# Kernel tuning notes

Hardware: AMD Instinct MI355X
Metric: run time of the kernel (lower is better)

## Reference

```python
import jax, jax.numpy as jnp
import numpy as np
import math

D = 1024
H = 16
HD = D // H  # 64
SCALE = math.sqrt(HD)


def setup_inputs() -> dict:
    key = jax.random.key(0)
    ks = jax.random.split(key, 4)
    B, S = 2, 2048
    x = jax.random.normal(ks[0], (B, S, D), dtype=jnp.float32)
    attention_mask = jnp.zeros((B, S), dtype=jnp.float32)  # additive mask
    w_attn = jax.random.normal(ks[1], (D, 3 * D), dtype=jnp.float32) * (1.0 / math.sqrt(D))
    b_attn = jnp.zeros((3 * D,), dtype=jnp.float32)
    w_proj = jax.random.normal(ks[2], (D, D), dtype=jnp.float32) * (1.0 / math.sqrt(D))
    b_proj = jnp.zeros((D,), dtype=jnp.float32)
    return {"x": x, "attention_mask": attention_mask, "w_attn": w_attn,
            "b_attn": b_attn, "w_proj": w_proj, "b_proj": b_proj}


def reference(x, attention_mask, w_attn, b_attn, w_proj, b_proj):
    B, S, _ = x.shape
    qkv = x @ w_attn + b_attn                      # [B,S,3D]
    q, k, v = jnp.split(qkv, 3, axis=-1)           # each [B,S,D]
    # split heads -> [B,H,S,HD]
    sh = lambda t: t.reshape(B, S, H, HD).transpose(0, 2, 1, 3)
    q, k, v = sh(q), sh(k), sh(v)
    scores = jnp.einsum('bhqd,bhkd->bhqk', q, k) / SCALE   # [B,H,S,S]
    scores = scores + attention_mask[:, None, None, :]      # additive mask [B,1,1,S]
    attn = jax.nn.softmax(scores, axis=-1)                  # dropout disabled (eval)
    out = jnp.einsum('bhqk,bhkd->bhqd', attn, v)            # [B,H,S,HD]
    out = out.transpose(0, 2, 1, 3).reshape(B, S, D)        # merge heads
    out = out @ w_proj + b_proj                              # resid dropout disabled
    return out
```

## Files before the change

kernel.cpp:

```cpp
#include <hip/hip_runtime.h>
#include <math.h>

#define B_  2
#define S_  2048
#define D_  1024
#define H_  16
#define HD_ 64
#define BS_ (B_ * S_)

typedef float f32x4 __attribute__((ext_vector_type(4)));
typedef int   i32x4 __attribute__((ext_vector_type(4)));

__device__ __forceinline__ float bf2f(unsigned short u) {
    union { unsigned int i; float f; } c; c.i = ((unsigned int)u) << 16; return c.f;
}
__device__ __forceinline__ unsigned short f2bf(float f) {
    union { float f; unsigned int i; } c; c.f = f;
    unsigned int r = c.i + 0x7FFFu + ((c.i >> 16) & 1u);
    return (unsigned short)(r >> 16);
}
__device__ __forceinline__ unsigned int cvtpk_bf16(float lo, float hi) {
    unsigned int r;
    asm volatile("v_cvt_pk_bf16_f32 %0, %1, %2" : "=v"(r) : "v"(lo), "v"(hi));
    return r;
}
__device__ __forceinline__ void gl_lds16(const void* g, void* l) {
    __builtin_amdgcn_global_load_lds((const __attribute__((address_space(1))) void*)g,
                                     (__attribute__((address_space(3))) void*)l, 16, 0, 0);
}
__device__ __forceinline__ void mfma_bf16(f32x4& d, i32x4 a, i32x4 b) {
    asm volatile("v_mfma_f32_16x16x32_bf16 %0, %1, %2, %0" : "+v"(d) : "v"(a), "v"(b));
}

__device__ __forceinline__ void transpose_tile64(
    const float* __restrict__ W, unsigned short* __restrict__ Wt,
    int K, int N, int bx, int by, float (*t)[65])
{
    const int n0 = bx * 64, k0 = by * 64;
    const int tx = threadIdx.x & 63, ty = threadIdx.x >> 6;
#pragma unroll
    for (int kk = 0; kk < 64; kk += 4)
        t[kk + ty][tx] = W[(size_t)(k0 + kk + ty) * N + n0 + tx];
    __syncthreads();
    const int nrow = threadIdx.x >> 2;
    const int kq   = (threadIdx.x & 3) * 4;
#pragma unroll
    for (int p = 0; p < 4; ++p) {
        const int k = p * 16 + kq;
        ushort4 v = make_ushort4(f2bf(t[k + 0][nrow]), f2bf(t[k + 1][nrow]),
                                 f2bf(t[k + 2][nrow]), f2bf(t[k + 3][nrow]));
        *reinterpret_cast<ushort4*>(Wt + (size_t)(n0 + nrow) * K + k0 + k) = v;
    }
}

__global__ __launch_bounds__(256) void prep_fused(
    const float* __restrict__ x,      unsigned short* __restrict__ xb,
    const float* __restrict__ w_attn, unsigned short* __restrict__ wat,
    const float* __restrict__ w_proj, unsigned short* __restrict__ wpt)
{
    __shared__ float t[64][65];
    const int bid = blockIdx.x;
    if (bid < 2048) {
        const int i = (bid * 256 + threadIdx.x) * 8;
        const float4 a = *reinterpret_cast<const float4*>(x + i);
        const float4 b = *reinterpret_cast<const float4*>(x + i + 4);
        ushort4 u0 = make_ushort4(f2bf(a.x), f2bf(a.y), f2bf(a.z), f2bf(a.w));
        ushort4 u1 = make_ushort4(f2bf(b.x), f2bf(b.y), f2bf(b.z), f2bf(b.w));
        *reinterpret_cast<ushort4*>(xb + i)     = u0;
        *reinterpret_cast<ushort4*>(xb + i + 4) = u1;
    } else if (bid < 2816) {
        const int tb = bid - 2048;
        transpose_tile64(w_attn, wat, D_, 3 * D_, tb % 48, tb / 48, t);
    } else {
        const int tb = bid - 2816;
        transpose_tile64(w_proj, wpt, D_, D_, tb & 15, tb >> 4, t);
    }
}

template <typename OutT, int BN>
__global__ __launch_bounds__(256) void gemm_bt_bf16(
    const unsigned short* __restrict__ A,
    const unsigned short* __restrict__ Bt,
    const float* __restrict__ bias,
    OutT* __restrict__ C, int M, int N, int K, int qcols)
{
    constexpr int NW = BN / 2;
    constexpr int NI = NW / 16;
    __shared__ alignas(16) unsigned short As[2][4096];
    __shared__ alignas(16) unsigned short Bs[2][BN * 32];

    const int tid  = threadIdx.x;
    const int wave = tid >> 6;
    const int l    = tid & 63;
    const int g    = l >> 4;
    const int r    = l & 15;
    const int wr   = wave >> 1, wc = wave & 1;

    const int nwg  = gridDim.x * gridDim.y;
    const int flat = blockIdx.x + gridDim.x * blockIdx.y;
    const int cpx  = nwg >> 3;
    const int swz  = (flat & 7) * cpx + (flat >> 3);
    const int bx   = swz % gridDim.x;
    const int by   = swz / gridDim.x;

    const int row0 = by * 128;
    const int col0 = bx * BN;
    const float sc = (col0 < qcols) ? 0.125f : 1.0f;

    const size_t aoff0 = (size_t)(row0 +   0 + l) * K + wave * 8;
    const size_t aoff1 = (size_t)(row0 +  64 + l) * K + wave * 8;
    const size_t boff0 = (size_t)(col0 +   0 + l) * K + wave * 8;
    const size_t boff1 = (size_t)(col0 +  64 + l) * K + wave * 8;

    auto stage = [&](int kt, int buf) {
        gl_lds16(A + aoff0 + kt, &As[buf][wave * 1024]);
        gl_lds16(A + aoff1 + kt, &As[buf][wave * 1024 + 512]);
        if constexpr (BN == 128) {
            gl_lds16(Bt + boff0 + kt, &Bs[buf][wave * 1024]);
            gl_lds16(Bt + boff1 + kt, &Bs[buf][wave * 1024 + 512]);
        } else {
            gl_lds16(Bt + boff0 + kt, &Bs[buf][wave * 512]);
        }
    };

    f32x4 acc[4][NI];
#pragma unroll
    for (int mi = 0; mi < 4; ++mi)
#pragma unroll
        for (int ni = 0; ni < NI; ++ni) acc[mi][ni] = (f32x4)0.f;

    stage(0, 0);
    __syncthreads();

    for (int kt = 0; kt < K; kt += 32) {
        const int cur = (kt >> 5) & 1;
        if (kt + 32 < K) stage(kt + 32, cur ^ 1);

        const unsigned short* Ab = &As[cur][g * 1024];
        const unsigned short* Bb = &Bs[cur][g * (BN * 8)];
        i32x4 af[4], bf[NI];
#pragma unroll
        for (int mi = 0; mi < 4; ++mi)
            af[mi] = *reinterpret_cast<const i32x4*>(Ab + (wr * 64 + mi * 16 + r) * 8);
#pragma unroll
        for (int ni = 0; ni < NI; ++ni)
            bf[ni] = *reinterpret_cast<const i32x4*>(Bb + (wc * NW + ni * 16 + r) * 8);
#pragma unroll
        for (int mi = 0; mi < 4; ++mi)
#pragma unroll
            for (int ni = 0; ni < NI; ++ni)
                mfma_bf16(acc[mi][ni], af[mi], bf[ni]);

        __syncthreads();
    }

#pragma unroll
    for (int ni = 0; ni < NI; ++ni) {
        const int n = col0 + wc * NW + ni * 16 + r;
        const float bv = bias[n];
#pragma unroll
        for (int mi = 0; mi < 4; ++mi) {
#pragma unroll
            for (int e = 0; e < 4; ++e) {
                const int m = row0 + wr * 64 + mi * 16 + g * 4 + e;
                const float val = (acc[mi][ni][e] + bv) * sc;
                if constexpr (sizeof(OutT) == 2)
                    C[(size_t)m * N + n] = (OutT)f2bf(val);
                else
                    C[(size_t)m * N + n] = (OutT)val;
            }
        }
    }
}

__global__ __launch_bounds__(512) void flash_attn_mfma(
    const unsigned short* __restrict__ qkv,
    const float* __restrict__ mask,
    unsigned short* __restrict__ out)
{
    __shared__ alignas(16) unsigned short Klds[2][4096];
    __shared__ alignas(16) unsigned short Vt[2][4096];

    const int tid  = threadIdx.x;
    const int wave = tid >> 6;
    const int l    = tid & 63;
    const int g    = l >> 4;
    const int r    = l & 15;

    const int flat = blockIdx.x + 16 * blockIdx.y + 256 * blockIdx.z;
    const int swz  = (flat & 7) * 64 + (flat >> 3);
    const int b    = swz >> 8;
    const int h    = (swz >> 4) & 15;
    const int q0   = (swz & 15) * 128;
    const int qw   = q0 + wave * 16;

    const size_t rs = 3 * (size_t)D_;
    const unsigned short* qb = qkv + (size_t)b * S_ * rs + (size_t)h * HD_;
    const unsigned short* kb = qb + D_;
    const unsigned short* vb = qb + 2 * D_;
    const float* mrow = mask + (size_t)b * S_;

    i32x4 qf[2];
#pragma unroll
    for (int ks = 0; ks < 2; ++ks)
        qf[ks] = *reinterpret_cast<const i32x4*>(
            qb + (size_t)(qw + r) * rs + ks * 32 + g * 8);

    const int kkey = (wave & 3) * 16 + (l >> 3);
    const int kuni = ((l & 7) ^ (l >> 3)) * 8;
    const int vkey = (wave & 3) * 16 + (l >> 2);
    const int vpart = l & 3;

    ushort4 vr[4];
    auto vload = [&](int kt) {
#pragma unroll
        for (int p = 0; p < 4; ++p)
            vr[p] = *reinterpret_cast<const ushort4*>(
                vb + (size_t)(kt + vkey) * rs + p * 16 + vpart * 4);
    };
    auto vwrite = [&](int buf) {
#pragma unroll
        for (int p = 0; p < 4; ++p) {
            const int d0 = p * 16 + vpart * 4;
            Vt[buf][(d0 + 0) * 64 + (vkey ^ (((d0 + 0) & 7) << 3))] = vr[p].x;
            Vt[buf][(d0 + 1) * 64 + (vkey ^ (((d0 + 1) & 7) << 3))] = vr[p].y;
            Vt[buf][(d0 + 2) * 64 + (vkey ^ (((d0 + 2) & 7) << 3))] = vr[p].z;
            Vt[buf][(d0 + 3) * 64 + (vkey ^ (((d0 + 3) & 7) << 3))] = vr[p].w;
        }
    };

    f32x4 acc[4];
    float m_i = -1e30f, l_i = 0.f;
#pragma unroll
    for (int mi = 0; mi < 4; ++mi) acc[mi] = (f32x4)0.f;

    if (wave < 4) {
        gl_lds16(kb + (size_t)(0 + kkey) * rs + kuni,     &Klds[0][(wave & 3) * 1024]);
        gl_lds16(kb + (size_t)(0 + kkey + 8) * rs + kuni, &Klds[0][(wave & 3) * 1024 + 512]);
    } else {
        vload(0);
        vwrite(0);
        vload(64);
    }
    __syncthreads();

    for (int kt = 0; kt < S_; kt += 64) {
        const int cur = (kt >> 6) & 1;
        if (wave < 4) {
            if (kt + 64 < S_) {
                gl_lds16(kb + (size_t)(kt + 64 + kkey) * rs + kuni,
                         &Klds[cur ^ 1][(wave & 3) * 1024]);
                gl_lds16(kb + (size_t)(kt + 64 + kkey + 8) * rs + kuni,
                         &Klds[cur ^ 1][(wave & 3) * 1024 + 512]);
            }
        } else {
            if (kt + 64 < S_) vwrite(cur ^ 1);
            if (kt + 128 < S_) vload(kt + 128);
        }

        const unsigned short* Kb = Klds[cur];
        const unsigned short* Vb = Vt[cur];

        f32x4 s[4];
#pragma unroll
        for (int mi = 0; mi < 4; ++mi) {
            const float4 mk = *reinterpret_cast<const float4*>(
                mrow + kt + mi * 16 + g * 4);
            s[mi][0] = mk.x; s[mi][1] = mk.y; s[mi][2] = mk.z; s[mi][3] = mk.w;
        }
#pragma unroll
        for (int ks = 0; ks < 2; ++ks)
#pragma unroll
            for (int mi = 0; mi < 4; ++mi) {
                const i32x4 kf = *reinterpret_cast<const i32x4*>(
                    Kb + (mi * 16 + r) * 64 + ((ks * 32 + g * 8) ^ ((r & 7) << 3)));
                mfma_bf16(s[mi], kf, qf[ks]);
            }

        float tmax = -1e30f;
#pragma unroll
        for (int mi = 0; mi < 4; ++mi)
#pragma unroll
            for (int e = 0; e < 4; ++e)
                tmax = fmaxf(tmax, s[mi][e]);
        tmax = fmaxf(tmax, __shfl_xor(tmax, 16));
        tmax = fmaxf(tmax, __shfl_xor(tmax, 32));
        const float mnew = fmaxf(m_i, tmax);
        const float corr = __expf(m_i - mnew);
        m_i = mnew;

        unsigned int pk[4][2];
        float ls = 0.f;
#pragma unroll
        for (int mi = 0; mi < 4; ++mi) {
            const float p0 = __expf(s[mi][0] - mnew);
            const float p1 = __expf(s[mi][1] - mnew);
            const float p2 = __expf(s[mi][2] - mnew);
            const float p3 = __expf(s[mi][3] - mnew);
            ls += (p0 + p1) + (p2 + p3);
            pk[mi][0] = cvtpk_bf16(p0, p1);
            pk[mi][1] = cvtpk_bf16(p2, p3);
        }
        l_i = l_i * corr + ls;
#pragma unroll
        for (int mi = 0; mi < 4; ++mi) acc[mi] *= corr;

#pragma unroll
        for (int ks = 0; ks < 2; ++ks) {
            i32x4 pf;
#pragma unroll
            for (int w = 0; w < 4; ++w) {
                const int src = (((g & 1) * 2 + (w >> 1)) << 4) + r;
                const unsigned int vA = __shfl(pk[2 * ks + 0][w & 1], src);
                const unsigned int vB = __shfl(pk[2 * ks + 1][w & 1], src);
                pf[w] = (int)((g >> 1) ? vB : vA);
            }
#pragma unroll
            for (int mi = 0; mi < 4; ++mi) {
                const i32x4 vf = *reinterpret_cast<const i32x4*>(
                    Vb + (mi * 16 + r) * 64 + ((ks * 32 + g * 8) ^ ((r & 7) << 3)));
                mfma_bf16(acc[mi], vf, pf);
            }
        }

        __syncthreads();
    }

    float lf = l_i;
    lf += __shfl_xor(lf, 16);
    lf += __shfl_xor(lf, 32);
    const float inv = 1.0f / lf;
    const size_t token = (size_t)b * S_ + qw + r;
#pragma unroll
    for (int mi = 0; mi < 4; ++mi) {
        const f32x4 v = acc[mi] * inv;
        uint2 w;
        w.x = cvtpk_bf16(v[0], v[1]);
        w.y = cvtpk_bf16(v[2], v[3]);
        *reinterpret_cast<uint2*>(
            out + token * D_ + h * HD_ + mi * 16 + g * 4) = w;
    }
}

extern "C" void kernel_launch(void* const* d_in, const int* in_sizes, int n_in,
                              void* d_out, int out_size, void* d_ws, size_t ws_size,
                              hipStream_t stream)
{
    const float* x      = (const float*)d_in[0];
    const float* amask  = (const float*)d_in[1];
    const float* w_attn = (const float*)d_in[2];
    const float* b_attn = (const float*)d_in[3];
    const float* w_proj = (const float*)d_in[4];
    const float* b_proj = (const float*)d_in[5];
    float* out = (float*)d_out;

    unsigned short* qkvb  = (unsigned short*)d_ws;
    unsigned short* attnb = qkvb  + (size_t)BS_ * 3 * D_;
    unsigned short* xb    = attnb + (size_t)BS_ * D_;
    unsigned short* wat   = xb    + (size_t)BS_ * D_;
    unsigned short* wpt   = wat   + (size_t)3 * D_ * D_;

    prep_fused<<<3072, 256, 0, stream>>>(x, xb, w_attn, wat, w_proj, wpt);

    gemm_bt_bf16<unsigned short, 128><<<dim3(3 * D_ / 128, BS_ / 128), 256, 0, stream>>>(
        xb, wat, b_attn, qkvb, BS_, 3 * D_, D_, D_);

    flash_attn_mfma<<<dim3(S_ / 128, H_, B_), 512, 0, stream>>>(qkvb, amask, attnb);

    gemm_bt_bf16<float, 64><<<dim3(D_ / 64, BS_ / 128), 256, 0, stream>>>(
        attnb, wpt, b_proj, out, BS_, D_, D_, 0);
}
```

Before: 167.4 us.

## Split attention KV range in halves and merge partial outputs with combine kernel

Flash attention now launches twice as many blocks, each processing half of the key/value sequence, writing normalized partial outputs plus per-row max and sum statistics into reused workspace (xb and wat buffers). A new combine kernel rescales and merges the two halves into the attention output before the projection GEMM. This aims to raise occupancy and parallelism on the many-CU GPU, where only 512 blocks existed before, at the cost of an extra kernel launch, extra memory traffic for the second partial output, and a second bf16 rounding step.

```diff
diff --git a/kernel.cpp b/kernel.cpp
--- a/kernel.cpp
+++ b/kernel.cpp
@@ -7,6 +7,7 @@
 #define H_  16
 #define HD_ 64
 #define BS_ (B_ * S_)
+#define SH_ (S_ / 2)
 
 typedef float f32x4 __attribute__((ext_vector_type(4)));
 typedef int   i32x4 __attribute__((ext_vector_type(4)));
@@ -173,10 +174,12 @@
     }
 }
 
-__global__ __launch_bounds__(512) void flash_attn_mfma(
+__global__ __launch_bounds__(512, 8) void flash_attn_split(
     const unsigned short* __restrict__ qkv,
     const float* __restrict__ mask,
-    unsigned short* __restrict__ out)
+    unsigned short* __restrict__ op0,
+    unsigned short* __restrict__ op1,
+    float2* __restrict__ ml)
 {
     __shared__ alignas(16) unsigned short Klds[2][4096];
     __shared__ alignas(16) unsigned short Vt[2][4096];
@@ -188,8 +191,11 @@
     const int r    = l & 15;
 
     const int flat = blockIdx.x + 16 * blockIdx.y + 256 * blockIdx.z;
-    const int swz  = (flat & 7) * 64 + (flat >> 3);
-    const int b    = swz >> 8;
+    const int swz  = (flat & 7) * 128 + (flat >> 3);
+    const int zz   = swz >> 8;
+    const int b    = zz >> 1;
+    const int half = zz & 1;
+    const int kv0  = half * SH_;
     const int h    = (swz >> 4) & 15;
     const int q0   = (swz & 15) * 128;
     const int qw   = q0 + wave * 16;
@@ -235,27 +241,27 @@
     for (int mi = 0; mi < 4; ++mi) acc[mi] = (f32x4)0.f;
 
     if (wave < 4) {
-        gl_lds16(kb + (size_t)(0 + kkey) * rs + kuni,     &Klds[0][(wave & 3) * 1024]);
-        gl_lds16(kb + (size_t)(0 + kkey + 8) * rs + kuni, &Klds[0][(wave & 3) * 1024 + 512]);
+        gl_lds16(kb + (size_t)(kv0 + kkey) * rs + kuni,     &Klds[0][(wave & 3) * 1024]);
+        gl_lds16(kb + (size_t)(kv0 + kkey + 8) * rs + kuni, &Klds[0][(wave & 3) * 1024 + 512]);
     } else {
-        vload(0);
+        vload(kv0);
         vwrite(0);
-        vload(64);
+        vload(kv0 + 64);
     }
     __syncthreads();
 
-    for (int kt = 0; kt < S_; kt += 64) {
-        const int cur = (kt >> 6) & 1;
+    for (int kt = kv0; kt < kv0 + SH_; kt += 64) {
+        const int cur = ((kt - kv0) >> 6) & 1;
         if (wave < 4) {
-            if (kt + 64 < S_) {
+            if (kt + 64 < kv0 + SH_) {
                 gl_lds16(kb + (size_t)(kt + 64 + kkey) * rs + kuni,
                          &Klds[cur ^ 1][(wave & 3) * 1024]);
                 gl_lds16(kb + (size_t)(kt + 64 + kkey + 8) * rs + kuni,
                          &Klds[cur ^ 1][(wave & 3) * 1024 + 512]);
             }
         } else {
-            if (kt + 64 < S_) vwrite(cur ^ 1);
-            if (kt + 128 < S_) vload(kt + 128);
+            if (kt + 64 < kv0 + SH_) vwrite(cur ^ 1);
+            if (kt + 128 < kv0 + SH_) vload(kt + 128);
         }
 
         const unsigned short* Kb = Klds[cur];
@@ -331,6 +337,7 @@
     lf += __shfl_xor(lf, 32);
     const float inv = 1.0f / lf;
     const size_t token = (size_t)b * S_ + qw + r;
+    unsigned short* obase = half ? op1 : op0;
 #pragma unroll
     for (int mi = 0; mi < 4; ++mi) {
         const f32x4 v = acc[mi] * inv;
@@ -338,8 +345,51 @@
         w.x = cvtpk_bf16(v[0], v[1]);
         w.y = cvtpk_bf16(v[2], v[3]);
         *reinterpret_cast<uint2*>(
-            out + token * D_ + h * HD_ + mi * 16 + g * 4) = w;
-    }
+            obase + token * D_ + h * HD_ + mi * 16 + g * 4) = w;
+    }
+    if (l < 16) {
+        const size_t mli = (((size_t)half * B_ + b) * H_ + h) * S_ + qw + l;
+        ml[mli] = make_float2(m_i, lf);
+    }
+}
+
+__global__ __launch_bounds__(256) void combine_halves(
+    unsigned short* o0,
+    const unsigned short* __restrict__ o1,
+    const float2* __restrict__ ml)
+{
+    const int gid   = blockIdx.x * 256 + threadIdx.x;
+    const int chunk = gid & 127;
+    const int token = gid >> 7;
+    const int h     = chunk >> 3;
+    const int b     = token >> 11;
+    const int q     = token & 2047;
+
+    const size_t mli = (((size_t)b) * H_ + h) * S_ + q;
+    const float2 a0 = ml[mli];
+    const float2 a1 = ml[(size_t)B_ * H_ * S_ + mli];
+    const float M  = fmaxf(a0.x, a1.x);
+    float w0 = a0.y * __expf(a0.x - M);
+    float w1 = a1.y * __expf(a1.x - M);
+    const float inv = 1.0f / (w0 + w1);
+    w0 *= inv; w1 *= inv;
+
+    const size_t off = (size_t)token * D_ + chunk * 8;
+    const ushort4 x0 = *reinterpret_cast<const ushort4*>(o0 + off);
+    const ushort4 x1 = *reinterpret_cast<const ushort4*>(o0 + off + 4);
+    const ushort4 y0 = *reinterpret_cast<const ushort4*>(o1 + off);
+    const ushort4 y1 = *reinterpret_cast<const ushort4*>(o1 + off + 4);
+    ushort4 r0, r1;
+    r0.x = f2bf(w0 * bf2f(x0.x) + w1 * bf2f(y0.x));
+    r0.y = f2bf(w0 * bf2f(x0.y) + w1 * bf2f(y0.y));
+    r0.z = f2bf(w0 * bf2f(x0.z) + w1 * bf2f(y0.z));
+    r0.w = f2bf(w0 * bf2f(x0.w) + w1 * bf2f(y0.w));
+    r1.x = f2bf(w0 * bf2f(x1.x) + w1 * bf2f(y1.x));
+    r1.y = f2bf(w0 * bf2f(x1.y) + w1 * bf2f(y1.y));
+    r1.z = f2bf(w0 * bf2f(x1.z) + w1 * bf2f(y1.z));
+    r1.w = f2bf(w0 * bf2f(x1.w) + w1 * bf2f(y1.w));
+    *reinterpret_cast<ushort4*>(o0 + off)     = r0;
+    *reinterpret_cast<ushort4*>(o0 + off + 4) = r1;
 }
 
 extern "C" void kernel_launch(void* const* d_in, const int* in_sizes, int n_in,
@@ -359,13 +409,17 @@
     unsigned short* xb    = attnb + (size_t)BS_ * D_;
     unsigned short* wat   = xb    + (size_t)BS_ * D_;
     unsigned short* wpt   = wat   + (size_t)3 * D_ * D_;
+    float2*         mlbuf = (float2*)wat;
 
     prep_fused<<<3072, 256, 0, stream>>>(x, xb, w_attn, wat, w_proj, wpt);
 
     gemm_bt_bf16<unsigned short, 128><<<dim3(3 * D_ / 128, BS_ / 128), 256, 0, stream>>>(
         xb, wat, b_attn, qkvb, BS_, 3 * D_, D_, D_);
 
-    flash_attn_mfma<<<dim3(S_ / 128, H_, B_), 512, 0, stream>>>(qkvb, amask, attnb);
+    flash_attn_split<<<dim3(S_ / 128, H_, B_ * 2), 512, 0, stream>>>(
+        qkvb, amask, attnb, xb, mlbuf);
+
+    combine_halves<<<(BS_ * D_ / 8) / 256, 256, 0, stream>>>(attnb, xb, mlbuf);
 
     gemm_bt_bf16<float, 64><<<dim3(D_ / 64, BS_ / 128), 256, 0, stream>>>(
         attnb, wpt, b_proj, out, BS_, D_, D_, 0);
```

Result: slower. 273.6 us, median of 2 (+63.4%).
